# Performance work log

Measured on AMD Instinct MI355X. Metric: run time of the kernel, lower is better.

The kernel has to match this reference:

```python
import jax, jax.numpy as jnp
import numpy as np

N_NODES = 50000
N_EDGES = 800000
F_IN = 128
HIDDEN = 32
HEADS = 4
F_OUT = 64
NEG_SLOPE = 0.2


def setup_inputs() -> dict:
    key = jax.random.key(0)
    ks = jax.random.split(key, 9)
    x = jax.random.normal(ks[0], (N_NODES, F_IN), dtype=jnp.float32)
    edge_index = jax.random.randint(ks[1], (2, N_EDGES), 0, N_NODES, dtype=jnp.int64)
    edge_weight = jax.random.uniform(ks[2], (N_EDGES,), dtype=jnp.float32)
    # GATConv parameters
    W = jax.random.normal(ks[3], (F_IN, HEADS * HIDDEN), dtype=jnp.float32) * (1.0 / np.sqrt(F_IN))
    a_src = jax.random.normal(ks[4], (HEADS, HIDDEN), dtype=jnp.float32) * 0.1
    a_dst = jax.random.normal(ks[5], (HEADS, HIDDEN), dtype=jnp.float32) * 0.1
    bias = jnp.zeros((HEADS * HIDDEN,), dtype=jnp.float32)
    # output linear
    W2 = jax.random.normal(ks[6], (HEADS * HIDDEN, F_OUT), dtype=jnp.float32) * (1.0 / np.sqrt(HEADS * HIDDEN))
    b2 = jnp.zeros((F_OUT,), dtype=jnp.float32)
    return {"x": x, "edge_index": edge_index, "edge_weight": edge_weight,
            "W": W, "a_src": a_src, "a_dst": a_dst, "bias": bias,
            "W2": W2, "b2": b2}


def reference(x, edge_index, edge_weight, W, a_src, a_dst, bias, W2, b2):
    src, dst = edge_index[0], edge_index[1]
    # linear transform per head: [N, H, C]
    h = (x @ W).reshape(-1, HEADS, HIDDEN)
    # per-node attention logits: [N, H]
    alpha_s = jnp.einsum('nhc,hc->nh', h, a_src)
    alpha_d = jnp.einsum('nhc,hc->nh', h, a_dst)
    # per-edge scores: [E, H]
    e = alpha_s[src] + alpha_d[dst]
    e = jnp.where(e >= 0, e, NEG_SLOPE * e)  # LeakyReLU(0.2)
    # segment softmax over destination neighborhoods
    m = jax.ops.segment_max(e, dst, num_segments=N_NODES)  # [N, H]
    ex = jnp.exp(e - m[dst])
    denom = jax.ops.segment_sum(ex, dst, num_segments=N_NODES)  # [N, H]
    alpha = ex / (denom[dst] + 1e-16)  # [E, H]
    # weighted scatter-add aggregation: [N, H, C]
    msgs = alpha[:, :, None] * h[src]
    out = jax.ops.segment_sum(msgs, dst, num_segments=N_NODES)
    out = out.reshape(-1, HEADS * HIDDEN) + bias
    out = jax.nn.elu(out)
    return out @ W2 + b2
```

## Files before the change

kernel.cpp:

```cpp
#include <hip/hip_runtime.h>

#define N_NODES 50000
#define N_EDGES 800000
#define F_IN 128
#define HH 128
#define HEADS 4
#define F_OUT 64
#define NEG_SLOPE 0.2f

#define NBIN ((N_NODES + 63) / 64)
#define XC 8
#define CAPXB 256
#define NCUR (NBIN * XC)
#define BINCAP (XC * CAPXB)

#define NODE_BLOCKS ((N_NODES + 31) / 32)
#define FILLB (N_EDGES / 256)
#define TOTAL_BLOCKS (NODE_BLOCKS + FILLB)
#define ZERO_BLOCKS ((NCUR + 255) / 256)

typedef __attribute__((ext_vector_type(8))) short short8v;
typedef __attribute__((ext_vector_type(4))) float float4v;

__device__ __forceinline__ unsigned short f2bf(float f) {
    unsigned int u = __float_as_uint(f);
    u = (u + 0x7FFFu + ((u >> 16) & 1u)) >> 16;
    return (unsigned short)u;
}
__device__ __forceinline__ float bf2f(unsigned short s) {
    return __uint_as_float((unsigned int)s << 16);
}

__global__ __launch_bounds__(256) void k_prep(
    const float* __restrict__ W, const float* __restrict__ a_src,
    const float* __restrict__ a_dst,
    unsigned short* __restrict__ Wf, unsigned short* __restrict__ Waf,
    int* __restrict__ cursor)
{
    const int b = blockIdx.x;
    const int t = threadIdx.x;

    if (b >= 9) {
        int i = (b - 9) * 256 + t;
        if (i < NCUR) cursor[i] = 0;
        return;
    }

    if (b < 8) {
        const int ks = b >> 1, nn = b & 1;
        const int w = t >> 6, lane = t & 63, l15 = lane & 15, l4 = lane >> 4;
        const int c  = w * 32 + nn * 16 + l15;
        const int kb = ks * 32 + l4 * 8;
        short8v frag;
        #pragma unroll
        for (int j = 0; j < 8; ++j)
            frag[j] = (short)f2bf(W[(size_t)(kb + j) * HH + c]);
        *(short8v*)&Wf[(size_t)((ks * 2 + nn) * 256 + t) * 8] = frag;
        return;
    }

    __shared__ float Wa[F_IN][8];
    #pragma unroll
    for (int i = 0; i < 4; ++i) {
        int idx = t * 4 + i;
        int k = idx >> 3, col = idx & 7;
        const float* av = (col < 4) ? a_src : a_dst;
        int hd = col & 3;
        float s = 0.f;
        #pragma unroll
        for (int cc = 0; cc < 32; ++cc)
            s = fmaf(W[(size_t)k * HH + hd * 32 + cc], av[hd * 32 + cc], s);
        Wa[k][col] = s;
    }
    __syncthreads();

    if (t < 64) {
        const int l15 = t & 15, l4 = t >> 4;
        #pragma unroll
        for (int ks = 0; ks < 4; ++ks) {
            short8v frag;
            #pragma unroll
            for (int j = 0; j < 8; ++j)
                frag[j] = (l15 < 8) ? (short)f2bf(Wa[ks * 32 + l4 * 8 + j][l15]) : (short)0;
            *(short8v*)&Waf[(size_t)(ks * 64 + t) * 8] = frag;
        }
    }
}

__global__ __launch_bounds__(256) void k_node_fill(
    const float* __restrict__ x,
    const unsigned short* __restrict__ Wf, const unsigned short* __restrict__ Waf,
    unsigned short* __restrict__ h_bf,
    float* __restrict__ as_out, float* __restrict__ ad_out,
    const int* __restrict__ ei, int* __restrict__ cursor, unsigned int* __restrict__ bins)
{
    __shared__ __align__(16) unsigned short xs[32][136];

    const int g = blockIdx.x;
    if (g % 3 != 0) {
        const int fidx = g - g / 3 - 1;
        if (fidx < FILLB) {
            const int vx = g & 7;
            int e = fidx * 256 + threadIdx.x;
            int S = ei[e];
            int D = ei[N_EDGES + e];
            int idx = (D >> 6) * XC + vx;
            int sl = atomicAdd(&cursor[idx], 1);
            if (sl < CAPXB)
                bins[(size_t)idx * CAPXB + sl] =
                    ((unsigned int)S << 6) | (unsigned int)(D & 63);
        }
        return;
    }

    const int tid  = threadIdx.x;
    const int base = (g / 3) * 32;
    const int w    = tid >> 6;
    const int lane = tid & 63;
    const int l15  = lane & 15;
    const int l4   = lane >> 4;

    short8v bfrag[4][2], wafrag[4];
    #pragma unroll
    for (int ks = 0; ks < 4; ++ks) {
        bfrag[ks][0] = *(const short8v*)&Wf[(size_t)((ks * 2 + 0) * 256 + tid) * 8];
        bfrag[ks][1] = *(const short8v*)&Wf[(size_t)((ks * 2 + 1) * 256 + tid) * 8];
        wafrag[ks]   = *(const short8v*)&Waf[(size_t)(ks * 64 + lane) * 8];
    }

    for (int i = tid; i < 32 * 32; i += 256) {
        int r = i >> 5, c4 = i & 31;
        int n = base + r;
        float4 v = (n < N_NODES) ? *(const float4*)&x[(size_t)n * F_IN + c4 * 4]
                                 : make_float4(0.f, 0.f, 0.f, 0.f);
        ushort4 hv;
        hv.x = f2bf(v.x); hv.y = f2bf(v.y); hv.z = f2bf(v.z); hv.w = f2bf(v.w);
        *(ushort4*)&xs[r][c4 * 4] = hv;
    }
    __syncthreads();

    float4v acc[2][2] = {};
    float4v accL[2] = {};
    #pragma unroll
    for (int ks = 0; ks < 4; ++ks) {
        short8v a0 = *(const short8v*)&xs[l15][ks * 32 + l4 * 8];
        short8v a1 = *(const short8v*)&xs[16 + l15][ks * 32 + l4 * 8];
        acc[0][0] = __builtin_amdgcn_mfma_f32_16x16x32_bf16(a0, bfrag[ks][0], acc[0][0], 0, 0, 0);
        acc[0][1] = __builtin_amdgcn_mfma_f32_16x16x32_bf16(a0, bfrag[ks][1], acc[0][1], 0, 0, 0);
        acc[1][0] = __builtin_amdgcn_mfma_f32_16x16x32_bf16(a1, bfrag[ks][0], acc[1][0], 0, 0, 0);
        acc[1][1] = __builtin_amdgcn_mfma_f32_16x16x32_bf16(a1, bfrag[ks][1], acc[1][1], 0, 0, 0);
        accL[0]   = __builtin_amdgcn_mfma_f32_16x16x32_bf16(a0, wafrag[ks], accL[0], 0, 0, 0);
        accL[1]   = __builtin_amdgcn_mfma_f32_16x16x32_bf16(a1, wafrag[ks], accL[1], 0, 0, 0);
    }

    if (w == 0 && l15 < 8) {
        #pragma unroll
        for (int m = 0; m < 2; ++m) {
            #pragma unroll
            for (int reg = 0; reg < 4; ++reg) {
                int node = base + m * 16 + l4 * 4 + reg;
                if (node >= N_NODES) continue;
                float lg = accL[m][reg];
                if (l15 < 4) as_out[node * HEADS + l15]       = lg;
                else         ad_out[node * HEADS + (l15 - 4)] = lg;
            }
        }
    }

    __syncthreads();
    #pragma unroll
    for (int m = 0; m < 2; ++m) {
        #pragma unroll
        for (int reg = 0; reg < 4; ++reg) {
            int r = m * 16 + l4 * 4 + reg;
            xs[r][w * 32 + l15]      = f2bf(acc[m][0][reg]);
            xs[r][w * 32 + 16 + l15] = f2bf(acc[m][1][reg]);
        }
    }
    __syncthreads();
    for (int i = tid; i < 32 * 16; i += 256) {
        int r = i >> 4, c8 = i & 15;
        int n = base + r;
        if (n < N_NODES)
            *(short8v*)&h_bf[(size_t)n * HH + c8 * 8] = *(const short8v*)&xs[r][c8 * 8];
    }
}

__global__ __launch_bounds__(256) void k_sort(
    const int* __restrict__ cursor, const unsigned int* __restrict__ bins,
    unsigned short* __restrict__ srcs_g, int2* __restrict__ offdeg)
{
    __shared__ unsigned int stg[BINCAP];
    __shared__ int lcnt[64], loff[64], lcur[64];
    __shared__ int scnt[XC], soff[XC], tot_s;

    const int bin = blockIdx.x;
    const int tid = threadIdx.x;

    if (tid < 64) { lcnt[tid] = 0; lcur[tid] = 0; }
    if (tid < XC) {
        int c = cursor[bin * XC + tid];
        scnt[tid] = c < CAPXB ? c : CAPXB;
    }
    __syncthreads();
    if (tid == 0) {
        int r = 0;
        #pragma unroll
        for (int j = 0; j < XC; ++j) { soff[j] = r; r += scnt[j]; }
        tot_s = r;
    }
    __syncthreads();
    #pragma unroll
    for (int sg = 0; sg < XC; ++sg) {
        int c = scnt[sg], o = soff[sg];
        const unsigned int* bp = &bins[(size_t)(bin * XC + sg) * CAPXB];
        for (int i = tid; i < c; i += 256) {
            unsigned int u = bp[i];
            stg[o + i] = u;
            atomicAdd(&lcnt[u & 63], 1);
        }
    }
    __syncthreads();
    if (tid < 64) {
        int v = lcnt[tid];
        int acc = v;
        #pragma unroll
        for (int off = 1; off < 64; off <<= 1) {
            int other = __shfl_up(acc, off, 64);
            if (tid >= off) acc += other;
        }
        loff[tid] = acc - v;
    }
    __syncthreads();
    const int tot = tot_s;
    for (int i = tid; i < tot; i += 256) {
        unsigned int u = stg[i];
        int d = u & 63;
        int sl = loff[d] + atomicAdd(&lcur[d], 1);
        srcs_g[(size_t)bin * BINCAP + sl] = (unsigned short)(u >> 6);
    }
    if (tid < 64) {
        int n = bin * 64 + tid;
        if (n < N_NODES)
            offdeg[n] = make_int2(bin * BINCAP + loff[tid], lcnt[tid]);
    }
}

__global__ __launch_bounds__(256) void k_gather(
    const int2* __restrict__ offdeg, const unsigned short* __restrict__ srcs_g,
    const float* __restrict__ as_, const float* __restrict__ ad_,
    const unsigned short* __restrict__ h_bf, unsigned short* __restrict__ agg_bf)
{
    int gid = blockIdx.x * 256 + threadIdx.x;
    int n = gid >> 6;
    if (n >= N_NODES) return;
    const int lane = gid & 63;
    const int hd  = lane >> 4;
    const int e16 = lane & 15;

    const float advv = ad_[n * 4 + hd];
    const int2 od = offdeg[n];
    const unsigned short* brow = &srcs_g[od.x];
    const int deg = od.y;

    float accx = 0.f, accy = 0.f, sum = 0.f;

    for (int cb = 0; cb < deg; cb += 16) {
        int m = deg - cb; if (m > 16) m = 16;
        int s = 0; float exown = 0.f;
        if (e16 < m) {
            s = brow[cb + e16];
            float lg = as_[s * 4 + hd] + advv;
            lg = lg >= 0.f ? lg : NEG_SLOPE * lg;
            exown = __expf(lg);
        }

#define GAT_BODY(j)                                                            \
        {                                                                      \
            float al = __shfl(exown, (hd << 4) + (j));                         \
            int   sj = __shfl(s,     (hd << 4) + (j));                         \
            unsigned int hv = *(const unsigned int*)&h_bf[(size_t)sj * HH + lane * 2]; \
            sum += al;                                                         \
            accx = fmaf(al, __uint_as_float((hv & 0xFFFFu) << 16), accx);      \
            accy = fmaf(al, __uint_as_float(hv & 0xFFFF0000u), accy);          \
        }

        if (m == 16) {
            #pragma unroll
            for (int j = 0; j < 16; ++j) GAT_BODY(j)
        } else {
            for (int j = 0; j < m; ++j) GAT_BODY(j)
        }
#undef GAT_BODY
    }

    float inv = 1.f / (sum + 1e-16f);
    unsigned int packed = (unsigned int)f2bf(accx * inv)
                        | ((unsigned int)f2bf(accy * inv) << 16);
    *(unsigned int*)&agg_bf[(size_t)n * HH + lane * 2] = packed;
}

__global__ __launch_bounds__(256) void k_output(
    const unsigned short* __restrict__ agg_bf, const float* __restrict__ bias,
    const float* __restrict__ W2, const float* __restrict__ b2,
    float* __restrict__ out)
{
    __shared__ float eb[64][132];

    const int tid  = threadIdx.x;
    const int base = blockIdx.x * 64;

    for (int i = tid; i < 64 * 16; i += 256) {
        int r = i >> 4, c8 = i & 15;
        int n = base + r;
        float v[8];
        if (n < N_NODES) {
            ushort4 p0 = *(const ushort4*)&agg_bf[(size_t)n * HH + c8 * 8];
            ushort4 p1 = *(const ushort4*)&agg_bf[(size_t)n * HH + c8 * 8 + 4];
            v[0] = bf2f(p0.x); v[1] = bf2f(p0.y); v[2] = bf2f(p0.z); v[3] = bf2f(p0.w);
            v[4] = bf2f(p1.x); v[5] = bf2f(p1.y); v[6] = bf2f(p1.z); v[7] = bf2f(p1.w);
        } else {
            #pragma unroll
            for (int j = 0; j < 8; ++j) v[j] = 0.f;
        }
        #pragma unroll
        for (int j = 0; j < 8; ++j) {
            float t = v[j] + bias[c8 * 8 + j];
            eb[r][c8 * 8 + j] = t > 0.f ? t : __expf(t) - 1.f;
        }
    }
    __syncthreads();

    const int cg = tid & 15;
    const int q  = tid >> 4;

    float4 b2v = *(const float4*)&b2[cg * 4];
    float4 acc[4] = { b2v, b2v, b2v, b2v };
    for (int k4 = 0; k4 < 32; ++k4) {
        const float* wr = &W2[(k4 * 4) * F_OUT + cg * 4];
        float4 w0 = *(const float4*)(wr);
        float4 w1 = *(const float4*)(wr + F_OUT);
        float4 w2 = *(const float4*)(wr + 2 * F_OUT);
        float4 w3 = *(const float4*)(wr + 3 * F_OUT);
        #pragma unroll
        for (int j = 0; j < 4; ++j) {
            float4 xv = *(const float4*)&eb[q * 4 + j][k4 * 4];
            acc[j].x = fmaf(xv.x, w0.x, acc[j].x); acc[j].y = fmaf(xv.x, w0.y, acc[j].y);
            acc[j].z = fmaf(xv.x, w0.z, acc[j].z); acc[j].w = fmaf(xv.x, w0.w, acc[j].w);
            acc[j].x = fmaf(xv.y, w1.x, acc[j].x); acc[j].y = fmaf(xv.y, w1.y, acc[j].y);
            acc[j].z = fmaf(xv.y, w1.z, acc[j].z); acc[j].w = fmaf(xv.y, w1.w, acc[j].w);
            acc[j].x = fmaf(xv.z, w2.x, acc[j].x); acc[j].y = fmaf(xv.z, w2.y, acc[j].y);
            acc[j].z = fmaf(xv.z, w2.z, acc[j].z); acc[j].w = fmaf(xv.z, w2.w, acc[j].w);
            acc[j].x = fmaf(xv.w, w3.x, acc[j].x); acc[j].y = fmaf(xv.w, w3.y, acc[j].y);
            acc[j].z = fmaf(xv.w, w3.z, acc[j].z); acc[j].w = fmaf(xv.w, w3.w, acc[j].w);
        }
    }
    #pragma unroll
    for (int j = 0; j < 4; ++j) {
        int n = base + q * 4 + j;
        if (n < N_NODES)
            *(float4*)&out[(size_t)n * F_OUT + cg * 4] = acc[j];
    }
}

extern "C" void kernel_launch(void* const* d_in, const int* in_sizes, int n_in,
                              void* d_out, int out_size, void* d_ws, size_t ws_size,
                              hipStream_t stream)
{
    const float* x     = (const float*)d_in[0];
    const int*   ei    = (const int*)  d_in[1];
    const float* W     = (const float*)d_in[3];
    const float* a_src = (const float*)d_in[4];
    const float* a_dst = (const float*)d_in[5];
    const float* bias  = (const float*)d_in[6];
    const float* W2    = (const float*)d_in[7];
    const float* b2    = (const float*)d_in[8];
    float* out = (float*)d_out;

    char* ws = (char*)d_ws;
    unsigned short* Wf   = (unsigned short*)ws;
    unsigned short* Waf  = Wf + 8 * 256 * 8;
    unsigned short* h_bf = Waf + 4 * 64 * 8;
    float* as_   = (float*)(h_bf + (size_t)N_NODES * HH);
    float* ad_   = as_ + (size_t)N_NODES * HEADS;
    int*   cursor= (int*)(ad_ + (size_t)N_NODES * HEADS);
    unsigned int* bins = (unsigned int*)(cursor + 6400);
    unsigned short* srcs_g = (unsigned short*)(bins + (size_t)NBIN * BINCAP);
    int2*  offdeg = (int2*)(srcs_g + (size_t)NBIN * BINCAP);
    unsigned short* agg_bf = (unsigned short*)(offdeg + N_NODES + 2);

    k_prep<<<9 + ZERO_BLOCKS, 256, 0, stream>>>(W, a_src, a_dst, Wf, Waf, cursor);
    k_node_fill<<<TOTAL_BLOCKS, 256, 0, stream>>>(
        x, Wf, Waf, h_bf, as_, ad_, ei, cursor, bins);
    k_sort<<<NBIN, 256, 0, stream>>>(cursor, bins, srcs_g, offdeg);
    k_gather<<<(N_NODES * 64 + 255) / 256, 256, 0, stream>>>(
        offdeg, srcs_g, as_, ad_, h_bf, agg_bf);
    k_output<<<(N_NODES + 63) / 64, 256, 0, stream>>>(agg_bf, bias, W2, b2, out);
}
```

Baseline: 126.3 us.

## Fuse output ELU and linear projection into gather kernel via wave shuffles

Removes the separate output kernel and the bf16 intermediate aggregate buffer. Each wave, which owns one node after aggregation, now applies bias and ELU in registers, then computes the 64-wide output projection by broadcasting the 128 activations with shuffles and reading W2 per lane. This saves one launch and the write and re-read of the aggregate. In exchange, W2 is re-read from cache by every node, with 128 shuffles plus FMAs per wave, and there is no shared-memory tiling across nodes. Separately, the weight-fragment loads in the node kernel are moved after the x staging barrier, which may reduce register pressure.

```diff
diff --git a/kernel.cpp b/kernel.cpp
--- a/kernel.cpp
+++ b/kernel.cpp
@@ -26,9 +26,6 @@
     unsigned int u = __float_as_uint(f);
     u = (u + 0x7FFFu + ((u >> 16) & 1u)) >> 16;
     return (unsigned short)u;
-}
-__device__ __forceinline__ float bf2f(unsigned short s) {
-    return __uint_as_float((unsigned int)s << 16);
 }
 
 __global__ __launch_bounds__(256) void k_prep(
@@ -120,14 +117,6 @@
     const int l15  = lane & 15;
     const int l4   = lane >> 4;
 
-    short8v bfrag[4][2], wafrag[4];
-    #pragma unroll
-    for (int ks = 0; ks < 4; ++ks) {
-        bfrag[ks][0] = *(const short8v*)&Wf[(size_t)((ks * 2 + 0) * 256 + tid) * 8];
-        bfrag[ks][1] = *(const short8v*)&Wf[(size_t)((ks * 2 + 1) * 256 + tid) * 8];
-        wafrag[ks]   = *(const short8v*)&Waf[(size_t)(ks * 64 + lane) * 8];
-    }
-
     for (int i = tid; i < 32 * 32; i += 256) {
         int r = i >> 5, c4 = i & 31;
         int n = base + r;
@@ -138,6 +127,14 @@
         *(ushort4*)&xs[r][c4 * 4] = hv;
     }
     __syncthreads();
+
+    short8v bfrag[4][2], wafrag[4];
+    #pragma unroll
+    for (int ks = 0; ks < 4; ++ks) {
+        bfrag[ks][0] = *(const short8v*)&Wf[(size_t)((ks * 2 + 0) * 256 + tid) * 8];
+        bfrag[ks][1] = *(const short8v*)&Wf[(size_t)((ks * 2 + 1) * 256 + tid) * 8];
+        wafrag[ks]   = *(const short8v*)&Waf[(size_t)(ks * 64 + lane) * 8];
+    }
 
     float4v acc[2][2] = {};
     float4v accL[2] = {};
@@ -246,10 +243,12 @@
     }
 }
 
-__global__ __launch_bounds__(256) void k_gather(
+__global__ __launch_bounds__(256) void k_gather_out(
     const int2* __restrict__ offdeg, const unsigned short* __restrict__ srcs_g,
     const float* __restrict__ as_, const float* __restrict__ ad_,
-    const unsigned short* __restrict__ h_bf, unsigned short* __restrict__ agg_bf)
+    const unsigned short* __restrict__ h_bf,
+    const float* __restrict__ bias, const float* __restrict__ W2,
+    const float* __restrict__ b2, float* __restrict__ out)
 {
     int gid = blockIdx.x * 256 + threadIdx.x;
     int n = gid >> 6;
@@ -295,72 +294,20 @@
     }
 
     float inv = 1.f / (sum + 1e-16f);
-    unsigned int packed = (unsigned int)f2bf(accx * inv)
-                        | ((unsigned int)f2bf(accy * inv) << 16);
-    *(unsigned int*)&agg_bf[(size_t)n * HH + lane * 2] = packed;
-}
-
-__global__ __launch_bounds__(256) void k_output(
-    const unsigned short* __restrict__ agg_bf, const float* __restrict__ bias,
-    const float* __restrict__ W2, const float* __restrict__ b2,
-    float* __restrict__ out)
-{
-    __shared__ float eb[64][132];
-
-    const int tid  = threadIdx.x;
-    const int base = blockIdx.x * 64;
-
-    for (int i = tid; i < 64 * 16; i += 256) {
-        int r = i >> 4, c8 = i & 15;
-        int n = base + r;
-        float v[8];
-        if (n < N_NODES) {
-            ushort4 p0 = *(const ushort4*)&agg_bf[(size_t)n * HH + c8 * 8];
-            ushort4 p1 = *(const ushort4*)&agg_bf[(size_t)n * HH + c8 * 8 + 4];
-            v[0] = bf2f(p0.x); v[1] = bf2f(p0.y); v[2] = bf2f(p0.z); v[3] = bf2f(p0.w);
-            v[4] = bf2f(p1.x); v[5] = bf2f(p1.y); v[6] = bf2f(p1.z); v[7] = bf2f(p1.w);
-        } else {
-            #pragma unroll
-            for (int j = 0; j < 8; ++j) v[j] = 0.f;
-        }
-        #pragma unroll
-        for (int j = 0; j < 8; ++j) {
-            float t = v[j] + bias[c8 * 8 + j];
-            eb[r][c8 * 8 + j] = t > 0.f ? t : __expf(t) - 1.f;
-        }
-    }
-    __syncthreads();
-
-    const int cg = tid & 15;
-    const int q  = tid >> 4;
-
-    float4 b2v = *(const float4*)&b2[cg * 4];
-    float4 acc[4] = { b2v, b2v, b2v, b2v };
-    for (int k4 = 0; k4 < 32; ++k4) {
-        const float* wr = &W2[(k4 * 4) * F_OUT + cg * 4];
-        float4 w0 = *(const float4*)(wr);
-        float4 w1 = *(const float4*)(wr + F_OUT);
-        float4 w2 = *(const float4*)(wr + 2 * F_OUT);
-        float4 w3 = *(const float4*)(wr + 3 * F_OUT);
-        #pragma unroll
-        for (int j = 0; j < 4; ++j) {
-            float4 xv = *(const float4*)&eb[q * 4 + j][k4 * 4];
-            acc[j].x = fmaf(xv.x, w0.x, acc[j].x); acc[j].y = fmaf(xv.x, w0.y, acc[j].y);
-            acc[j].z = fmaf(xv.x, w0.z, acc[j].z); acc[j].w = fmaf(xv.x, w0.w, acc[j].w);
-            acc[j].x = fmaf(xv.y, w1.x, acc[j].x); acc[j].y = fmaf(xv.y, w1.y, acc[j].y);
-            acc[j].z = fmaf(xv.y, w1.z, acc[j].z); acc[j].w = fmaf(xv.y, w1.w, acc[j].w);
-            acc[j].x = fmaf(xv.z, w2.x, acc[j].x); acc[j].y = fmaf(xv.z, w2.y, acc[j].y);
-            acc[j].z = fmaf(xv.z, w2.z, acc[j].z); acc[j].w = fmaf(xv.z, w2.w, acc[j].w);
-            acc[j].x = fmaf(xv.w, w3.x, acc[j].x); acc[j].y = fmaf(xv.w, w3.y, acc[j].y);
-            acc[j].z = fmaf(xv.w, w3.z, acc[j].z); acc[j].w = fmaf(xv.w, w3.w, acc[j].w);
-        }
-    }
-    #pragma unroll
-    for (int j = 0; j < 4; ++j) {
-        int n = base + q * 4 + j;
-        if (n < N_NODES)
-            *(float4*)&out[(size_t)n * F_OUT + cg * 4] = acc[j];
-    }
+    float e0 = accx * inv + bias[lane * 2];
+    float e1 = accy * inv + bias[lane * 2 + 1];
+    e0 = e0 > 0.f ? e0 : __expf(e0) - 1.f;
+    e1 = e1 > 0.f ? e1 : __expf(e1) - 1.f;
+
+    float o = b2[lane];
+    #pragma unroll
+    for (int k4 = 0; k4 < 64; ++k4) {
+        float v0 = __shfl(e0, k4);
+        float v1 = __shfl(e1, k4);
+        o = fmaf(v0, W2[(size_t)(2 * k4)     * F_OUT + lane], o);
+        o = fmaf(v1, W2[(size_t)(2 * k4 + 1) * F_OUT + lane], o);
+    }
+    out[(size_t)n * F_OUT + lane] = o;
 }
 
 extern "C" void kernel_launch(void* const* d_in, const int* in_sizes, int n_in,
@@ -387,13 +334,11 @@
     unsigned int* bins = (unsigned int*)(cursor + 6400);
     unsigned short* srcs_g = (unsigned short*)(bins + (size_t)NBIN * BINCAP);
     int2*  offdeg = (int2*)(srcs_g + (size_t)NBIN * BINCAP);
-    unsigned short* agg_bf = (unsigned short*)(offdeg + N_NODES + 2);
 
     k_prep<<<9 + ZERO_BLOCKS, 256, 0, stream>>>(W, a_src, a_dst, Wf, Waf, cursor);
     k_node_fill<<<TOTAL_BLOCKS, 256, 0, stream>>>(
         x, Wf, Waf, h_bf, as_, ad_, ei, cursor, bins);
     k_sort<<<NBIN, 256, 0, stream>>>(cursor, bins, srcs_g, offdeg);
-    k_gather<<<(N_NODES * 64 + 255) / 256, 256, 0, stream>>>(
-        offdeg, srcs_g, as_, ad_, h_bf, agg_bf);
-    k_output<<<(N_NODES + 63) / 64, 256, 0, stream>>>(agg_bf, bias, W2, b2, out);
-}
+    k_gather_out<<<(N_NODES * 64 + 255) / 256, 256, 0, stream>>>(
+        offdeg, srcs_g, as_, ad_, h_bf, bias, W2, b2, out);
+}
```

New measurement: 152.2 us. 20.5% more time.
